# Kernel tuning notes

Measured on AMD Instinct MI355X. Metric: run time of the kernel, lower is better.

Reference implementation:

```python
import jax, jax.numpy as jnp
import numpy as np

DIM = 1024
STATE_DIM = 64
DT_RANK = 32
HEAD_DIM = 64
NUM_HEADS = 8
B, L = 4, 4096
INNER = NUM_HEADS * HEAD_DIM  # 512


def setup_inputs() -> dict:
    key = jax.random.key(0)
    ks = jax.random.split(key, 10)
    s = 0.02
    x = jax.random.normal(ks[0], (B, L, DIM), dtype=jnp.float32)
    W_sel = jax.random.normal(ks[1], (DIM, DT_RANK + 2 * STATE_DIM), dtype=jnp.float32) * s
    dt_W = jax.random.normal(ks[2], (DT_RANK, INNER), dtype=jnp.float32) * s
    dt_b = jnp.ones((INNER,), dtype=jnp.float32)  # nn.init.constant_(dt_proj.bias, 1.0)
    Wk = jax.random.normal(ks[3], (DIM, INNER), dtype=jnp.float32) * s
    Wv = jax.random.normal(ks[4], (DIM, INNER), dtype=jnp.float32) * s
    Wr = jax.random.normal(ks[5], (DIM, INNER), dtype=jnp.float32) * s
    Wg = jax.random.normal(ks[6], (DIM, INNER), dtype=jnp.float32) * s
    Wo = jax.random.normal(ks[7], (INNER, DIM), dtype=jnp.float32) * s
    # per-head decay rates: 0.1 + 2.9 * h/(H-1)
    rates = 0.1 + 2.9 * (jnp.arange(NUM_HEADS, dtype=jnp.float32) / (NUM_HEADS - 1))
    base_decay = jnp.broadcast_to(rates[:, None], (NUM_HEADS, HEAD_DIM)).astype(jnp.float32)
    time_first = jax.random.uniform(ks[8], (NUM_HEADS, HEAD_DIM), minval=-0.1, maxval=0.1, dtype=jnp.float32)
    return {"x": x, "W_sel": W_sel, "dt_W": dt_W, "dt_b": dt_b, "Wk": Wk, "Wv": Wv,
            "Wr": Wr, "Wg": Wg, "Wo": Wo, "base_decay": base_decay, "time_first": time_first}


def _scan_core(k, v, r, g, decay, bscale, time_first, state0):
    # k,v,r,g,decay: [B,L,H,Dh]; bscale: [B,L]; state0: [B,H,Dh,Dh]
    def step(st, inp):
        k_t, v_t, r_t, g_t, d_t, b_t = inp
        st = d_t[..., None] * st + b_t[:, None, None, None] * jnp.einsum('bhk,bhv->bhkv', k_t, v_t)
        wkv = jnp.einsum('bhkv,bhk->bhv', st, k_t) + time_first * k_t * v_t
        return st, r_t * wkv * g_t
    xs = tuple(jnp.moveaxis(a, 1, 0) for a in (k, v, r, g, decay)) + (bscale.T,)
    state, ys = jax.lax.scan(step, state0, xs)
    return jnp.moveaxis(ys, 0, 1), state  # [B,L,H,Dh], [B,H,Dh,Dh]


def reference(x, W_sel, dt_W, dt_b, Wk, Wv, Wr, Wg, Wo, base_decay, time_first):
    Bsz, Lq, D = x.shape
    proj = x @ W_sel
    dt_raw = proj[..., :DT_RANK]
    B_vec = proj[..., DT_RANK:DT_RANK + STATE_DIM]
    # C_vec = proj[..., DT_RANK+STATE_DIM:]  # computed but unused in original
    delta_t = jax.nn.softplus(dt_raw @ dt_W + dt_b).reshape(Bsz, Lq, NUM_HEADS, HEAD_DIM)
    k = (x @ Wk).reshape(Bsz, Lq, NUM_HEADS, HEAD_DIM)
    v = (x @ Wv).reshape(Bsz, Lq, NUM_HEADS, HEAD_DIM)
    r = jax.nn.sigmoid((x @ Wr).reshape(Bsz, Lq, NUM_HEADS, HEAD_DIM))
    g = jax.nn.sigmoid((x @ Wg).reshape(Bsz, Lq, NUM_HEADS, HEAD_DIM))
    decay = jnp.exp(-base_decay[None, None] * delta_t)
    bscale = B_vec.mean(axis=-1)  # [B,L]
    state0 = jnp.zeros((Bsz, NUM_HEADS, HEAD_DIM, HEAD_DIM), dtype=x.dtype)
    ys, state = _scan_core(k, v, r, g, decay, bscale, time_first, state0)
    output = ys.reshape(Bsz, Lq, INNER) @ Wo
    return output, state
```

## Files before the change

### kernel.cpp

```cpp
#include <hip/hip_runtime.h>
#include <hip/hip_bf16.h>
#include <stdint.h>

#define ROWS 16384
#define SEQ  4096
#define CT   16
#define NC   256
#define NBH  32

typedef __attribute__((ext_vector_type(8))) short bf16x8;
typedef __attribute__((ext_vector_type(4))) float f32x4;

__device__ __forceinline__ float bf2f(unsigned short u){
  unsigned int x = ((unsigned int)u) << 16;
  float f; __builtin_memcpy(&f, &x, 4); return f;
}
__device__ __forceinline__ unsigned short f2bf(float f){
  __hip_bfloat16 h = __float2bfloat16(f);
  unsigned short u; __builtin_memcpy(&u, &h, 2); return u;
}

__device__ __forceinline__ void gload16(const unsigned short* g, unsigned short* l){
  __builtin_amdgcn_global_load_lds((const __attribute__((address_space(1))) unsigned int*)g,
                                   (__attribute__((address_space(3))) unsigned int*)l, 16, 0, 0);
}


__global__ __launch_bounds__(256) void k_prep_x(const float* __restrict__ x,
                                                unsigned short* __restrict__ xbf){
  int id = blockIdx.x*256 + threadIdx.x;
  const float4* in = (const float4*)x;
  float4 a = in[(size_t)id*2], b = in[(size_t)id*2+1];
  union { unsigned short s[8]; uint4 v; } u;
  u.s[0]=f2bf(a.x); u.s[1]=f2bf(a.y); u.s[2]=f2bf(a.z); u.s[3]=f2bf(a.w);
  u.s[4]=f2bf(b.x); u.s[5]=f2bf(b.y); u.s[6]=f2bf(b.z); u.s[7]=f2bf(b.w);
  ((uint4*)xbf)[id] = u.v;
}

__global__ __launch_bounds__(256) void k_prep_dteff(const float* __restrict__ Wsel,
                                                    const float* __restrict__ dtW,
                                                    unsigned short* __restrict__ wcat){
  int id = blockIdx.x*256 + threadIdx.x;
  int n = id >> 10, kk = id & 1023;
  float acc = 0.f;
  #pragma unroll
  for(int j=0;j<32;j++) acc += Wsel[kk*160 + j] * dtW[j*512 + n];
  wcat[(size_t)n*1024 + kk] = f2bf(acc);
}

__global__ __launch_bounds__(256) void k_prep_wbs(const float* __restrict__ Wsel,
                                                  unsigned short* __restrict__ wcat){
  int kk = blockIdx.x*256 + threadIdx.x;
  float acc = 0.f;
  #pragma unroll
  for(int j=0;j<64;j++) acc += Wsel[kk*160 + 32 + j];
  wcat[(size_t)2560*1024 + kk] = f2bf(acc * (1.0f/64.0f));
}

__global__ __launch_bounds__(256) void k_transpose(const float* __restrict__ src,
                                                   unsigned short* __restrict__ dst,
                                                   int R, int C){
  __shared__ float tile[32][33];
  int tx = threadIdx.x & 31, ty = threadIdx.x >> 5;
  int r0 = blockIdx.x*32, c0 = blockIdx.y*32;
  #pragma unroll
  for(int i=0;i<4;i++) tile[ty+i*8][tx] = src[(size_t)(r0+ty+i*8)*C + c0+tx];
  __syncthreads();
  #pragma unroll
  for(int i=0;i<4;i++) dst[(size_t)(c0+ty+i*8)*R + r0+tx] = f2bf(tile[tx][ty+i*8]);
}

template<int MODE>
__global__ __launch_bounds__(256) void k_gemm(const unsigned short* __restrict__ A,
                                              const unsigned short* __restrict__ B,
                                              int K, int ncols,
                                              float* __restrict__ dtbuf,
                                              unsigned short* __restrict__ kvbuf,
                                              unsigned short* __restrict__ rgbuf,
                                              float* __restrict__ lastbuf,
                                              float* __restrict__ cout){
  __shared__ __align__(16) unsigned short As[128*64];
  __shared__ __align__(16) unsigned short Bs[128*64];
  const int tid = threadIdx.x, w = tid>>6, l = tid&63;

  int orig = blockIdx.x;
  int q = gridDim.x >> 3;
  int swz = (orig & 7)*q + (orig >> 3);
  const int row0 = (swz / ncols)*128, col0 = (swz % ncols)*128;

  const int wm = w & 1, wn = w >> 1;
  f32x4 acc[4][4];
  #pragma unroll
  for(int i=0;i<4;i++)
    #pragma unroll
    for(int j=0;j<4;j++){ f32x4 z = {0.f,0.f,0.f,0.f}; acc[i][j] = z; }

  const int nk = K >> 6;
  const int lr = l >> 3;
  const int lc = ((l & 7) ^ lr) * 8;

  for(int kt=0; kt<nk; ++kt){
    __syncthreads();
    #pragma unroll
    for(int i=0;i<4;i++){
      int r = w*32 + i*8;
      gload16(&A[(size_t)(row0 + r + lr)*K + kt*64 + lc], &As[r*64]);
      gload16(&B[(size_t)(col0 + r + lr)*K + kt*64 + lc], &Bs[r*64]);
    }
    asm volatile("s_waitcnt vmcnt(0)");
    __syncthreads();
    #pragma unroll
    for(int kk=0;kk<2;kk++){
      bf16x8 af[4], bfr[4];
      const int pb = (kk*64 + (l>>4)*16) ^ ((l&7)<<4);
      #pragma unroll
      for(int mf=0;mf<4;mf++){
        int row = wm*64 + mf*16 + (l&15);
        af[mf] = *(const bf16x8*)((const char*)As + row*128 + pb);
      }
      #pragma unroll
      for(int nf=0;nf<4;nf++){
        int row = wn*64 + nf*16 + (l&15);
        bfr[nf] = *(const bf16x8*)((const char*)Bs + row*128 + pb);
      }
      #pragma unroll
      for(int mf=0;mf<4;mf++)
        #pragma unroll
        for(int nf=0;nf<4;nf++)
          acc[mf][nf] = __builtin_amdgcn_mfma_f32_16x16x32_bf16(af[mf], bfr[nf], acc[mf][nf], 0,0,0);
    }
  }
  #pragma unroll
  for(int mf=0;mf<4;mf++)
    #pragma unroll
    for(int nf=0;nf<4;nf++)
      #pragma unroll
      for(int j=0;j<4;j++){
        int gr = row0 + wm*64 + mf*16 + (l>>4)*4 + j;
        int gc = col0 + wn*64 + nf*16 + (l&15);
        float v = acc[mf][nf][j];
        if(MODE == 1){
          cout[(size_t)gr*1024 + gc] = v;
        } else {
          if(col0 < 512)        dtbuf[(size_t)gr*512  + gc]        = v;
          else if(col0 < 1536)  kvbuf[(size_t)gr*1024 + (gc-512)]  = f2bf(v);
          else if(col0 < 2560)  rgbuf[(size_t)gr*1024 + (gc-1536)] = f2bf(v);
          else if(gc == 2560)   lastbuf[gr] = v;
        }
      }
}

__global__ __launch_bounds__(64) void k_scan1(const float* __restrict__ dtbuf,
                                              const unsigned short* __restrict__ kvbuf,
                                              const float* __restrict__ lastbuf,
                                              const float* __restrict__ base_decay,
                                              const float* __restrict__ dt_b,
                                              const float* __restrict__ time_first,
                                              unsigned short* __restrict__ wsQ,
                                              unsigned short* __restrict__ wsI,
                                              unsigned short* __restrict__ wsU,
                                              float* __restrict__ wsA){
  const int bx = blockIdx.x;
  const int c = bx & (NC-1), bh = bx >> 8;
  const int b = bh >> 3, h = bh & 7;
  const int d = threadIdx.x;
  const int rowbase = b*SEQ + c*CT;
  const int hd = h*64 + d;

  __shared__ float vsm[16][68];
  __shared__ float qsm[16][68];
  __shared__ float ksm[16][68];
  __shared__ float Ps[16][20];
  __shared__ float bsL[16];

  const float rate = base_decay[hd], dtb = dt_b[hd], tfv = time_first[hd];

  float kreg[16], vreg[16], kb[16];
  float run = 0.f;
  #pragma unroll
  for(int t=0;t<16;t++){
    int row = rowbase + t;
    float xdt = dtbuf[(size_t)row*512 + hd] + dtb;
    float sp = (xdt > 30.f) ? xdt : log1pf(expf(xdt));
    run -= rate*sp;
    float ep = expf(run), em = expf(-run);
    kreg[t] = bf2f(kvbuf[(size_t)row*1024 + hd]);
    vreg[t] = bf2f(kvbuf[(size_t)row*1024 + 512 + hd]);
    float bs = lastbuf[row];
    float q  = kreg[t]*ep;
    float ks = kreg[t]*em;
    kb[t] = ks*bs;
    wsQ[(size_t)row*512 + hd] = f2bf(q);
    vsm[t][d] = vreg[t];
    qsm[t][d] = q;
    ksm[t][d] = ks;
    if(d == 0) bsL[t] = bs;
  }
  wsA[(size_t)bx*64 + d] = expf(run);
  __syncthreads();

  #pragma unroll 4
  for(int vc=0; vc<16; vc++){
    float u0=0,u1=0,u2=0,u3=0;
    #pragma unroll
    for(int t=0;t<16;t++){
      float4 v4 = *(const float4*)&vsm[t][vc*4];
      u0 += kb[t]*v4.x; u1 += kb[t]*v4.y; u2 += kb[t]*v4.z; u3 += kb[t]*v4.w;
    }
    size_t ub = (size_t)bx*4096 + (size_t)(vc*4)*64 + d;
    wsU[ub]       = f2bf(u0);
    wsU[ub+64]    = f2bf(u1);
    wsU[ub+128]   = f2bf(u2);
    wsU[ub+192]   = f2bf(u3);
  }

  {
    const int tt = d >> 2, s0 = d & 3;
    #pragma unroll
    for(int ss=0; ss<4; ss++){
      int s = s0 + ss*4;
      float dot = 0.f;
      #pragma unroll
      for(int dc=0; dc<16; dc++){
        float4 a4 = *(const float4*)&qsm[tt][dc*4];
        float4 b4 = *(const float4*)&ksm[s][dc*4];
        dot += a4.x*b4.x + a4.y*b4.y + a4.z*b4.z + a4.w*b4.w;
      }
      Ps[tt][s] = (s <= tt) ? dot*bsL[s] : 0.f;
    }
  }
  __syncthreads();

  #pragma unroll 1
  for(int t=0;t<16;t++){
    float acc = tfv*kreg[t]*vreg[t];
    #pragma unroll
    for(int s=0;s<16;s++) acc += Ps[t][s]*vreg[s];
    int row = rowbase + t;
    wsI[(size_t)row*512 + hd] = f2bf(acc);
  }
}

__global__ __launch_bounds__(256) void k_scan2(unsigned short* __restrict__ US,
                                               const float* __restrict__ wsA,
                                               float* __restrict__ outState){
  const int bh = blockIdx.x, vq = blockIdx.y;
  const int t = threadIdx.x;
  const int v = vq*16 + (t>>4);
  const int d0 = (t & 15)*4;
  const size_t ubase = (size_t)bh*NC*4096 + (size_t)v*64 + d0;
  const size_t abase = (size_t)bh*NC*64 + d0;
  float st0=0.f, st1=0.f, st2=0.f, st3=0.f;
  ushort4 ua[8], ub[8]; float4 aa[8], ab[8];
  #pragma unroll
  for(int i=0;i<8;i++){
    ua[i] = *(const ushort4*)&US[ubase + (size_t)i*4096];
    aa[i] = *(const float4*)&wsA[abase + (size_t)i*64];
  }
  for(int g=0; g<32; g+=2){
    #pragma unroll
    for(int i=0;i<8;i++){
      int c = (g+1)*8 + i;
      ub[i] = *(const ushort4*)&US[ubase + (size_t)c*4096];
      ab[i] = *(const float4*)&wsA[abase + (size_t)c*64];
    }
    #pragma unroll
    for(int i=0;i<8;i++){
      int c = g*8 + i;
      ushort4 sw; sw.x=f2bf(st0); sw.y=f2bf(st1); sw.z=f2bf(st2); sw.w=f2bf(st3);
      *(ushort4*)&US[ubase + (size_t)c*4096] = sw;
      st0 = aa[i].x*(st0 + bf2f(ua[i].x));
      st1 = aa[i].y*(st1 + bf2f(ua[i].y));
      st2 = aa[i].z*(st2 + bf2f(ua[i].z));
      st3 = aa[i].w*(st3 + bf2f(ua[i].w));
    }
    if(g+2 < 32){
      #pragma unroll
      for(int i=0;i<8;i++){
        int c = (g+2)*8 + i;
        ua[i] = *(const ushort4*)&US[ubase + (size_t)c*4096];
        aa[i] = *(const float4*)&wsA[abase + (size_t)c*64];
      }
    }
    #pragma unroll
    for(int i=0;i<8;i++){
      int c = (g+1)*8 + i;
      ushort4 sw; sw.x=f2bf(st0); sw.y=f2bf(st1); sw.z=f2bf(st2); sw.w=f2bf(st3);
      *(ushort4*)&US[ubase + (size_t)c*4096] = sw;
      st0 = ab[i].x*(st0 + bf2f(ub[i].x));
      st1 = ab[i].y*(st1 + bf2f(ub[i].y));
      st2 = ab[i].z*(st2 + bf2f(ub[i].z));
      st3 = ab[i].w*(st3 + bf2f(ub[i].w));
    }
  }
  #pragma unroll
  for(int j=0;j<4;j++)
    outState[(size_t)bh*4096 + (size_t)(d0+j)*64 + v] = (j==0)?st0:((j==1)?st1:((j==2)?st2:st3));
}

__global__ __launch_bounds__(64) void k_out(const unsigned short* __restrict__ wsQ,
                                            const unsigned short* __restrict__ wsI,
                                            const unsigned short* __restrict__ states,
                                            const unsigned short* __restrict__ rgbuf,
                                            unsigned short* __restrict__ ys){
  const int bx = blockIdx.x;
  const int c = bx & (NC-1), bh = bx >> 8;
  const int b = bh >> 3, h = bh & 7;
  const int lane = threadIdx.x;
  const int rowbase = b*SEQ + c*CT;
  __shared__ float qL[16][68];
  #pragma unroll
  for(int t=0;t<16;t++)
    qL[t][lane] = bf2f(wsQ[(size_t)(rowbase+t)*512 + h*64 + lane]);
  float stv[64];
  {
    const unsigned short* sp = &states[(size_t)bx*4096 + (size_t)lane*64];
    #pragma unroll
    for(int dd=0; dd<16; dd++){
      ushort4 u = *(const ushort4*)&sp[dd*4];
      stv[dd*4+0]=bf2f(u.x); stv[dd*4+1]=bf2f(u.y); stv[dd*4+2]=bf2f(u.z); stv[dd*4+3]=bf2f(u.w);
    }
  }
  __syncthreads();
  #pragma unroll 1
  for(int t=0;t<16;t++){
    float w = 0.f;
    #pragma unroll
    for(int dc=0; dc<16; dc++){
      float4 q4 = *(const float4*)&qL[t][dc*4];
      w += q4.x*stv[dc*4] + q4.y*stv[dc*4+1] + q4.z*stv[dc*4+2] + q4.w*stv[dc*4+3];
    }
    int row = rowbase + t;
    float intra = bf2f(wsI[(size_t)row*512 + h*64 + lane]);
    float rr = bf2f(rgbuf[(size_t)row*1024 + h*64 + lane]);
    float gg = bf2f(rgbuf[(size_t)row*1024 + 512 + h*64 + lane]);
    rr = 1.f/(1.f + expf(-rr));
    gg = 1.f/(1.f + expf(-gg));
    float y = rr*(w + intra)*gg;
    ys[(size_t)row*512 + h*64 + lane] = f2bf(y);
  }
}

extern "C" void kernel_launch(void* const* d_in, const int* in_sizes, int n_in,
                              void* d_out, int out_size, void* d_ws, size_t ws_size,
                              hipStream_t stream){
  const float* x          = (const float*)d_in[0];
  const float* W_sel      = (const float*)d_in[1];
  const float* dt_W       = (const float*)d_in[2];
  const float* dt_b       = (const float*)d_in[3];
  const float* Wk         = (const float*)d_in[4];
  const float* Wv         = (const float*)d_in[5];
  const float* Wr         = (const float*)d_in[6];
  const float* Wg         = (const float*)d_in[7];
  const float* Wo         = (const float*)d_in[8];
  const float* base_decay = (const float*)d_in[9];
  const float* time_first = (const float*)d_in[10];
  float* out = (float*)d_out;

  char* wsb = (char*)d_ws;
  unsigned short* Xbf   = (unsigned short*)(wsb + 0);
  unsigned short* wsQ   = (unsigned short*)(wsb + 0);
  unsigned short* wsI   = (unsigned short*)(wsb + 16777216);
  unsigned short* Wcat  = (unsigned short*)(wsb + 33554432);
  unsigned short* WoT   = (unsigned short*)(wsb + 39059456);
  float*          dtbuf = (float*)         (wsb + 40108032);
  unsigned short* ys    = (unsigned short*)(wsb + 40108032);
  unsigned short* kvbuf = (unsigned short*)(wsb + 73662464);
  unsigned short* rgbuf = (unsigned short*)(wsb + 107216896);
  float*          lastb = (float*)         (wsb + 140771328);
  unsigned short* wsU   = (unsigned short*)(wsb + 149159936);
  float*          wsA   = (float*)         (wsb + 216268800);

  k_prep_x<<<dim3(8192), dim3(256), 0, stream>>>(x, Xbf);
  k_prep_dteff<<<dim3(2048), dim3(256), 0, stream>>>(W_sel, dt_W, Wcat);
  k_transpose<<<dim3(32,16), dim3(256), 0, stream>>>(Wk, Wcat + (size_t)512*1024,  1024, 512);
  k_transpose<<<dim3(32,16), dim3(256), 0, stream>>>(Wv, Wcat + (size_t)1024*1024, 1024, 512);
  k_transpose<<<dim3(32,16), dim3(256), 0, stream>>>(Wr, Wcat + (size_t)1536*1024, 1024, 512);
  k_transpose<<<dim3(32,16), dim3(256), 0, stream>>>(Wg, Wcat + (size_t)2048*1024, 1024, 512);
  k_transpose<<<dim3(16,32), dim3(256), 0, stream>>>(Wo, WoT, 512, 1024);
  k_prep_wbs<<<dim3(4), dim3(256), 0, stream>>>(W_sel, Wcat);
  hipMemsetAsync(Wcat + (size_t)2561*1024, 0, (size_t)127*1024*2, stream);

  k_gemm<0><<<dim3(2688), dim3(256), 0, stream>>>(Xbf, Wcat, 1024, 21, dtbuf, kvbuf, rgbuf, lastb, nullptr);

  k_scan1<<<dim3(8192), dim3(64), 0, stream>>>(dtbuf, kvbuf, lastb, base_decay, dt_b, time_first,
                                               wsQ, wsI, wsU, wsA);
  k_scan2<<<dim3(32,4), dim3(256), 0, stream>>>(wsU, wsA, out + 16777216);
  k_out<<<dim3(8192), dim3(64), 0, stream>>>(wsQ, wsI, wsU, rgbuf, ys);

  k_gemm<1><<<dim3(1024), dim3(256), 0, stream>>>(ys, WoT, 512, 8, nullptr, nullptr, nullptr, nullptr, out);
}
```

Before: 511.3 us.

## Use bf16 MFMA for chunk scan intra/update products and output state contraction

Rewrites the per-chunk scan kernel so the q·k^T attention-like matrix, the k^T v state update and the intra-chunk P·v product all run as 16x16x32 bf16 MFMA instructions, staging operands in padded bf16 LDS tiles with zero-padding for the K dimension. The output kernel likewise loads q and the chunk-start states into LDS with vectorized loads and contracts them with MFMA instead of scalar FMA loops. This removes heavy scalar FP32 FMA and LDS traffic, at the cost of extra bf16 rounding of intermediates (q, ks, v, kb, P) and a scattered, less-coalesced global store pattern for wsU, wsI and ys.

```diff
diff --git a/kernel.cpp b/kernel.cpp
--- a/kernel.cpp
+++ b/kernel.cpp
@@ -163,14 +163,16 @@
   const int bx = blockIdx.x;
   const int c = bx & (NC-1), bh = bx >> 8;
   const int b = bh >> 3, h = bh & 7;
-  const int d = threadIdx.x;
+  const int l = threadIdx.x;
   const int rowbase = b*SEQ + c*CT;
-  const int hd = h*64 + d;
-
-  __shared__ float vsm[16][68];
-  __shared__ float qsm[16][68];
-  __shared__ float ksm[16][68];
-  __shared__ float Ps[16][20];
+  const int hd = h*64 + l;
+
+  __shared__ __align__(16) unsigned short q_t [16*72];
+  __shared__ __align__(16) unsigned short ks_t[16*72];
+  __shared__ __align__(16) unsigned short vt  [64*40];
+  __shared__ __align__(16) unsigned short kbt [64*40];
+  __shared__ __align__(16) unsigned short p_t [16*40];
+  __shared__ float tft[16*68];
   __shared__ float bsL[16];
 
   const float rate = base_decay[hd], dtb = dt_b[hd], tfv = time_first[hd];
@@ -187,58 +189,101 @@
     kreg[t] = bf2f(kvbuf[(size_t)row*1024 + hd]);
     vreg[t] = bf2f(kvbuf[(size_t)row*1024 + 512 + hd]);
     float bs = lastbuf[row];
-    float q  = kreg[t]*ep;
+    float qv  = kreg[t]*ep;
     float ks = kreg[t]*em;
     kb[t] = ks*bs;
-    wsQ[(size_t)row*512 + hd] = f2bf(q);
-    vsm[t][d] = vreg[t];
-    qsm[t][d] = q;
-    ksm[t][d] = ks;
-    if(d == 0) bsL[t] = bs;
-  }
-  wsA[(size_t)bx*64 + d] = expf(run);
+    unsigned short qb = f2bf(qv);
+    wsQ[(size_t)row*512 + hd] = qb;
+    q_t [t*72 + l] = qb;
+    ks_t[t*72 + l] = f2bf(ks);
+    if(l == 0) bsL[t] = bs;
+  }
+  wsA[(size_t)bx*64 + l] = expf(run);
+
+  #pragma unroll
+  for(int t=0;t<16;t++) tft[t*68 + l] = tfv*kreg[t]*vreg[t];
+
+  {
+    union { unsigned short s[16]; uint4 v4[2]; } pv, pk;
+    #pragma unroll
+    for(int t=0;t<16;t++){ pv.s[t]=f2bf(vreg[t]); pk.s[t]=f2bf(kb[t]); }
+    uint4 z = {0,0,0,0};
+    *(uint4*)&vt [l*40 + 0]  = pv.v4[0];
+    *(uint4*)&vt [l*40 + 8]  = pv.v4[1];
+    *(uint4*)&vt [l*40 + 16] = z;
+    *(uint4*)&vt [l*40 + 24] = z;
+    *(uint4*)&kbt[l*40 + 0]  = pk.v4[0];
+    *(uint4*)&kbt[l*40 + 8]  = pk.v4[1];
+    *(uint4*)&kbt[l*40 + 16] = z;
+    *(uint4*)&kbt[l*40 + 24] = z;
+    if(l < 32){
+      int rr = l >> 1, hh = l & 1;
+      *(uint4*)&p_t[rr*40 + 16 + hh*8] = z;
+    }
+  }
   __syncthreads();
 
-  #pragma unroll 4
-  for(int vc=0; vc<16; vc++){
-    float u0=0,u1=0,u2=0,u3=0;
-    #pragma unroll
-    for(int t=0;t<16;t++){
-      float4 v4 = *(const float4*)&vsm[t][vc*4];
-      u0 += kb[t]*v4.x; u1 += kb[t]*v4.y; u2 += kb[t]*v4.z; u3 += kb[t]*v4.w;
-    }
-    size_t ub = (size_t)bx*4096 + (size_t)(vc*4)*64 + d;
-    wsU[ub]       = f2bf(u0);
-    wsU[ub+64]    = f2bf(u1);
-    wsU[ub+128]   = f2bf(u2);
-    wsU[ub+192]   = f2bf(u3);
-  }
-
   {
-    const int tt = d >> 2, s0 = d & 3;
-    #pragma unroll
-    for(int ss=0; ss<4; ss++){
-      int s = s0 + ss*4;
-      float dot = 0.f;
-      #pragma unroll
-      for(int dc=0; dc<16; dc++){
-        float4 a4 = *(const float4*)&qsm[tt][dc*4];
-        float4 b4 = *(const float4*)&ksm[s][dc*4];
-        dot += a4.x*b4.x + a4.y*b4.y + a4.z*b4.z + a4.w*b4.w;
+    f32x4 accP = {0.f,0.f,0.f,0.f};
+    #pragma unroll
+    for(int kc=0;kc<2;kc++){
+      bf16x8 a  = *(const bf16x8*)&q_t [(l&15)*72 + kc*32 + (l>>4)*8];
+      bf16x8 bb = *(const bf16x8*)&ks_t[(l&15)*72 + kc*32 + (l>>4)*8];
+      accP = __builtin_amdgcn_mfma_f32_16x16x32_bf16(a, bb, accP, 0,0,0);
+    }
+    const int s = l & 15;
+    const float bss = bsL[s];
+    #pragma unroll
+    for(int r=0;r<4;r++){
+      int t = (l>>4)*4 + r;
+      float pv = (s <= t) ? accP[r]*bss : 0.f;
+      p_t[t*40 + s] = f2bf(pv);
+    }
+  }
+  __syncthreads();
+
+  bf16x8 va[4], kbb[4];
+  #pragma unroll
+  for(int i=0;i<4;i++){
+    va[i]  = *(const bf16x8*)&vt [(i*16 + (l&15))*40 + (l>>4)*8];
+    kbb[i] = *(const bf16x8*)&kbt[(i*16 + (l&15))*40 + (l>>4)*8];
+  }
+  f32x4 accU[4][4];
+  #pragma unroll
+  for(int vr=0;vr<4;vr++)
+    #pragma unroll
+    for(int dc=0;dc<4;dc++){
+      f32x4 z = {0.f,0.f,0.f,0.f};
+      accU[vr][dc] = __builtin_amdgcn_mfma_f32_16x16x32_bf16(va[vr], kbb[dc], z, 0,0,0);
+    }
+  f32x4 accI[4];
+  {
+    bf16x8 ap = *(const bf16x8*)&p_t[(l&15)*40 + (l>>4)*8];
+    #pragma unroll
+    for(int vc=0;vc<4;vc++){
+      f32x4 z = {0.f,0.f,0.f,0.f};
+      accI[vc] = __builtin_amdgcn_mfma_f32_16x16x32_bf16(ap, va[vc], z, 0,0,0);
+    }
+  }
+  #pragma unroll
+  for(int vr=0;vr<4;vr++)
+    #pragma unroll
+    for(int dc=0;dc<4;dc++)
+      #pragma unroll
+      for(int r=0;r<4;r++){
+        int v = vr*16 + (l>>4)*4 + r;
+        int d = dc*16 + (l&15);
+        wsU[(size_t)bx*4096 + (size_t)v*64 + d] = f2bf(accU[vr][dc][r]);
       }
-      Ps[tt][s] = (s <= tt) ? dot*bsL[s] : 0.f;
-    }
-  }
-  __syncthreads();
-
-  #pragma unroll 1
-  for(int t=0;t<16;t++){
-    float acc = tfv*kreg[t]*vreg[t];
-    #pragma unroll
-    for(int s=0;s<16;s++) acc += Ps[t][s]*vreg[s];
-    int row = rowbase + t;
-    wsI[(size_t)row*512 + hd] = f2bf(acc);
-  }
+  #pragma unroll
+  for(int vc=0;vc<4;vc++)
+    #pragma unroll
+    for(int r=0;r<4;r++){
+      int t = (l>>4)*4 + r;
+      int v = vc*16 + (l&15);
+      float val = accI[vc][r] + tft[t*68 + v];
+      wsI[(size_t)(rowbase+t)*512 + h*64 + v] = f2bf(val);
+    }
 }
 
 __global__ __launch_bounds__(256) void k_scan2(unsigned short* __restrict__ US,
@@ -306,39 +351,54 @@
   const int bx = blockIdx.x;
   const int c = bx & (NC-1), bh = bx >> 8;
   const int b = bh >> 3, h = bh & 7;
-  const int lane = threadIdx.x;
+  const int l = threadIdx.x;
   const int rowbase = b*SEQ + c*CT;
-  __shared__ float qL[16][68];
-  #pragma unroll
-  for(int t=0;t<16;t++)
-    qL[t][lane] = bf2f(wsQ[(size_t)(rowbase+t)*512 + h*64 + lane]);
-  float stv[64];
-  {
-    const unsigned short* sp = &states[(size_t)bx*4096 + (size_t)lane*64];
-    #pragma unroll
-    for(int dd=0; dd<16; dd++){
-      ushort4 u = *(const ushort4*)&sp[dd*4];
-      stv[dd*4+0]=bf2f(u.x); stv[dd*4+1]=bf2f(u.y); stv[dd*4+2]=bf2f(u.z); stv[dd*4+3]=bf2f(u.w);
-    }
+
+  __shared__ __align__(16) unsigned short q_l [16*72];
+  __shared__ __align__(16) unsigned short st_l[64*72];
+
+  #pragma unroll
+  for(int i=0;i<2;i++){
+    int idx = i*64 + l, t = idx>>3, c8 = idx&7;
+    uint4 val = *(const uint4*)&wsQ[(size_t)(rowbase+t)*512 + h*64 + c8*8];
+    *(uint4*)&q_l[t*72 + c8*8] = val;
+  }
+  #pragma unroll
+  for(int i=0;i<8;i++){
+    int idx = i*64 + l, v = idx>>3, c8 = idx&7;
+    uint4 val = *(const uint4*)&states[(size_t)bx*4096 + (size_t)idx*8];
+    *(uint4*)&st_l[v*72 + c8*8] = val;
   }
   __syncthreads();
-  #pragma unroll 1
-  for(int t=0;t<16;t++){
-    float w = 0.f;
-    #pragma unroll
-    for(int dc=0; dc<16; dc++){
-      float4 q4 = *(const float4*)&qL[t][dc*4];
-      w += q4.x*stv[dc*4] + q4.y*stv[dc*4+1] + q4.z*stv[dc*4+2] + q4.w*stv[dc*4+3];
-    }
-    int row = rowbase + t;
-    float intra = bf2f(wsI[(size_t)row*512 + h*64 + lane]);
-    float rr = bf2f(rgbuf[(size_t)row*1024 + h*64 + lane]);
-    float gg = bf2f(rgbuf[(size_t)row*1024 + 512 + h*64 + lane]);
-    rr = 1.f/(1.f + expf(-rr));
-    gg = 1.f/(1.f + expf(-gg));
-    float y = rr*(w + intra)*gg;
-    ys[(size_t)row*512 + h*64 + lane] = f2bf(y);
-  }
+
+  f32x4 acc[4];
+  #pragma unroll
+  for(int vc=0;vc<4;vc++){ f32x4 z = {0.f,0.f,0.f,0.f}; acc[vc] = z; }
+  #pragma unroll
+  for(int kc=0;kc<2;kc++){
+    bf16x8 a = *(const bf16x8*)&q_l[(l&15)*72 + kc*32 + (l>>4)*8];
+    #pragma unroll
+    for(int vc=0;vc<4;vc++){
+      bf16x8 bb = *(const bf16x8*)&st_l[(vc*16 + (l&15))*72 + kc*32 + (l>>4)*8];
+      acc[vc] = __builtin_amdgcn_mfma_f32_16x16x32_bf16(a, bb, acc[vc], 0,0,0);
+    }
+  }
+  #pragma unroll
+  for(int vc=0;vc<4;vc++)
+    #pragma unroll
+    for(int r=0;r<4;r++){
+      int t = (l>>4)*4 + r;
+      int v = vc*16 + (l&15);
+      size_t row = (size_t)(rowbase + t);
+      float w = acc[vc][r];
+      float intra = bf2f(wsI[row*512 + h*64 + v]);
+      float rr = bf2f(rgbuf[row*1024 + h*64 + v]);
+      float gg = bf2f(rgbuf[row*1024 + 512 + h*64 + v]);
+      rr = 1.f/(1.f + expf(-rr));
+      gg = 1.f/(1.f + expf(-gg));
+      float y = rr*(w + intra)*gg;
+      ys[row*512 + h*64 + v] = f2bf(y);
+    }
 }
 
 extern "C" void kernel_launch(void* const* d_in, const int* in_sizes, int n_in,
```

After: 465.7 us. -8.9%, faster.
